# Performance work log

Measured on AMD Instinct MI355X. Metric: run time of the kernel, lower is better.

## Reference

```python
import jax, jax.numpy as jnp
import numpy as np

B, Hdim, Wdim, C = 8, 128, 128, 64
HEADS, R, EXP = 1, 8, 4
HID = C * EXP
EPS = 1e-5

def layernorm(x, g, b):
    m = jnp.mean(x, -1, keepdims=True)
    v = jnp.mean((x - m) ** 2, -1, keepdims=True)
    return (x - m) * jax.lax.rsqrt(v + EPS) * g + b

def setup_inputs() -> dict:
    key = jax.random.key(0)
    ks = jax.random.split(key, 16)
    s = 0.02
    inp = {
        'x': jax.random.normal(ks[0], (B, Hdim * Wdim, C), jnp.float32),
        'H': Hdim, 'W': Wdim,
        'ln1_g': jnp.ones((C,)), 'ln1_b': jnp.zeros((C,)),
        'q_w': jax.random.normal(ks[1], (C, C)) * s, 'q_b': jnp.zeros((C,)),
        'kv_w': jax.random.normal(ks[2], (C, 2 * C)) * s, 'kv_b': jnp.zeros((2 * C,)),
        'proj_w': jax.random.normal(ks[3], (C, C)) * s, 'proj_b': jnp.zeros((C,)),
        'sr_w': jax.random.normal(ks[4], (R, R, C, C)) * s, 'sr_b': jnp.zeros((C,)),
        'srn_g': jnp.ones((C,)), 'srn_b': jnp.zeros((C,)),
        'ln2_g': jnp.ones((C,)), 'ln2_b': jnp.zeros((C,)),
        'fc1_w': jax.random.normal(ks[5], (C, HID)) * s, 'fc1_b': jnp.zeros((HID,)),
        'dw_w': jax.random.normal(ks[6], (3, 3, 1, HID)) * s,  # depthwise HWIO
        'fc2_w': jax.random.normal(ks[7], (HID, C)) * s, 'fc2_b': jnp.zeros((C,)),
    }
    return inp

def reference(x, H, W, ln1_g, ln1_b, q_w, q_b, kv_w, kv_b, proj_w, proj_b,
              sr_w, sr_b, srn_g, srn_b, ln2_g, ln2_b, fc1_w, fc1_b, dw_w, fc2_w, fc2_b):
    Bq, N, Cq = x.shape
    hd = Cq // HEADS
    scale = hd ** -0.5
    # --- attention branch (dropout = identity in eval) ---
    h = layernorm(x, ln1_g, ln1_b)
    q = (h @ q_w + q_b).reshape(Bq, N, HEADS, hd)
    # spatial reduction: conv RxR stride R
    xr = h.reshape(Bq, H, W, Cq)
    xr = jax.lax.conv_general_dilated(xr, sr_w, (R, R), 'VALID',
                                      dimension_numbers=('NHWC', 'HWIO', 'NHWC')) + sr_b
    Nr = (H // R) * (W // R)
    xr = layernorm(xr.reshape(Bq, Nr, Cq), srn_g, srn_b)
    kv = (xr @ kv_w + kv_b).reshape(Bq, Nr, 2, HEADS, hd)
    k, v = kv[:, :, 0], kv[:, :, 1]  # [B,Nr,H,hd]
    attn = jnp.einsum('bnhd,bmhd->bhnm', q, k) * scale
    attn = jax.nn.softmax(attn, axis=-1)
    o = jnp.einsum('bhnm,bmhd->bnhd', attn, v).reshape(Bq, N, Cq)
    x = x + (o @ proj_w + proj_b)
    # --- Mix-FFN branch ---
    h2 = layernorm(x, ln2_g, ln2_b)
    f = h2 @ fc1_w + fc1_b  # [B,N,HID]
    f = f.reshape(Bq, H, W, HID)
    f = jax.lax.conv_general_dilated(f, dw_w, (1, 1), 'SAME',
                                     dimension_numbers=('NHWC', 'HWIO', 'NHWC'),
                                     feature_group_count=HID)
    f = jax.nn.gelu(f.reshape(Bq, N, HID), approximate=False)
    return x + (f @ fc2_w + fc2_b)
```

## Files before the change

kernel.cpp:

```cpp
#include <hip/hip_runtime.h>
#include <hip/hip_bf16.h>


typedef __hip_bfloat16 bf16;
typedef __attribute__((ext_vector_type(8))) short s8v;
typedef __attribute__((ext_vector_type(4))) float f4v;

#define N_TOK 16384
#define CDIM 64
#define NR 256
#define HID 256
#define EPS 1e-5f

__device__ __forceinline__ float b2f(bf16 v) { return __bfloat162float(v); }
__device__ __forceinline__ bf16 f2b(float v) { return __float2bfloat16(v); }
__device__ __forceinline__ short bfbits(float f) {
  bf16 h = __float2bfloat16(f);
  return __builtin_bit_cast(short, h);
}
__device__ __forceinline__ float bits2f(short s) {
  const unsigned u = ((unsigned)(unsigned short)s) << 16;
  return __builtin_bit_cast(float, u);
}
__device__ __forceinline__ float2 unpk(unsigned u) {
  const unsigned lo = u << 16;
  const unsigned hi = u & 0xffff0000u;
  float2 r;
  r.x = __builtin_bit_cast(float, lo);
  r.y = __builtin_bit_cast(float, hi);
  return r;
}

__device__ __forceinline__ float wred_sum(float v) {
#pragma unroll
  for (int o = 32; o >= 1; o >>= 1) v += __shfl_xor(v, o);
  return v;
}

__global__ __launch_bounds__(256) void k_prep(
    const float* __restrict__ qw, const float* __restrict__ pw,
    const float* __restrict__ w1, const float* __restrict__ w2,
    const float* __restrict__ srw,
    bf16* __restrict__ qwT, bf16* __restrict__ pwT,
    bf16* __restrict__ w1T, bf16* __restrict__ w2T,
    bf16* __restrict__ srwT) {
  int id = blockIdx.x * 256 + threadIdx.x;
  if (id < 4096) {
    const int n = id >> 6, k = id & 63;
    qwT[(n << 6) + ((((k >> 3) ^ (n & 7)) << 3)) + (k & 7)] = f2b(qw[(k << 6) + n]);
  } else if (id < 8192) {
    id -= 4096;
    const int n = id >> 6, k = id & 63;
    pwT[(n << 6) + ((((k >> 3) ^ (n & 7)) << 3)) + (k & 7)] = f2b(pw[(k << 6) + n]);
  } else if (id < 24576) {
    id -= 8192;
    const int n = id >> 6, k = id & 63;
    w1T[(n << 6) + ((((k >> 3) ^ (n & 7)) << 3)) + (k & 7)] = f2b(w1[(k << 8) + n]);
  } else if (id < 40960) {
    id -= 24576;
    const int n = id >> 8, k = id & 255;
    w2T[(n << 8) + ((((k >> 3) ^ (n & 7)) << 3)) + (k & 7)] = f2b(w2[(k << 6) + n]);
  } else {
    id -= 40960;
    const int n = id >> 12, k = id & 4095;
    srwT[(n << 12) + k] = f2b(srw[(k << 6) + n]);
  }
}

__global__ __launch_bounds__(256) void k_ln1(
    const float* __restrict__ x, const float* __restrict__ g, const float* __restrict__ bb,
    bf16* __restrict__ h) {
  const int tid = threadIdx.x;
  const int row = (blockIdx.x << 6) + (tid >> 2), q4 = tid & 3;
  const float4* xp = (const float4*)(x + (((size_t)row) << 6) + (q4 << 4));
  float v[16];
#pragma unroll
  for (int j4 = 0; j4 < 4; j4++) {
    const float4 a = xp[j4];
    v[j4 * 4 + 0] = a.x; v[j4 * 4 + 1] = a.y; v[j4 * 4 + 2] = a.z; v[j4 * 4 + 3] = a.w;
  }
  float s = 0.f;
#pragma unroll
  for (int j = 0; j < 16; j++) s += v[j];
  s += __shfl_xor(s, 1); s += __shfl_xor(s, 2);
  const float mean = s * (1.f / 64.f);
  float vs = 0.f;
#pragma unroll
  for (int j = 0; j < 16; j++) { v[j] -= mean; vs += v[j] * v[j]; }
  vs += __shfl_xor(vs, 1); vs += __shfl_xor(vs, 2);
  const float rs = rsqrtf(vs * (1.f / 64.f) + EPS);
  s8v p0, p1;
#pragma unroll
  for (int j = 0; j < 16; j++) {
    const int c = (q4 << 4) + j;
    const short hb = bfbits(v[j] * rs * g[c] + bb[c]);
    if (j < 8) p0[j] = hb; else p1[j - 8] = hb;
  }
  bf16* hp = h + (((size_t)row) << 6) + (q4 << 4);
  *(s8v*)hp = p0;
  *(s8v*)(hp + 8) = p1;
}

__global__ __launch_bounds__(256) void k_srgemm(
    const bf16* __restrict__ h, const bf16* __restrict__ srwT,
    float* __restrict__ part) {
  const int tid = threadIdx.x, lane = tid & 63, wv = tid >> 6;
  const int quad = lane >> 4, li = lane & 15;
  const int rt = blockIdx.x >> 3, ks = blockIdx.x & 7;
  const int g = (rt << 6) + (wv << 4) + li;
  const int b = g >> 8, pm = g & 255;
  const int py = pm >> 4, px = pm & 15;
  const int n0 = (py << 10) + (px << 3);
  const size_t abase = ((size_t)(b * N_TOK + n0)) << 6;

  f4v acc[4];
#pragma unroll
  for (int t = 0; t < 4; t++) acc[t] = (f4v){0.f, 0.f, 0.f, 0.f};

#pragma unroll
  for (int i = 0; i < 16; i++) {
    const int kk = (ks << 4) + i;
    const int sp = kk >> 1;
    const int nd = ((sp >> 3) << 7) + (sp & 7);
    const int ci = ((kk & 1) << 5) + (quad << 3);
    s8v av = *(const s8v*)(h + abase + (((size_t)nd) << 6) + ci);
    const int koff = (kk << 5) + (quad << 3);
#pragma unroll
    for (int t = 0; t < 4; t++) {
      s8v bv = *(const s8v*)(srwT + ((((t << 4) + li)) << 12) + koff);
      acc[t] = __builtin_amdgcn_mfma_f32_16x16x32_bf16(av, bv, acc[t], 0, 0, 0);
    }
  }
  float* pp = part + (((size_t)ks) << 17);
#pragma unroll
  for (int t = 0; t < 4; t++)
#pragma unroll
    for (int r = 0; r < 4; r++) {
      const int row = (rt << 6) + (wv << 4) + (quad << 2) + r;
      pp[(row << 6) + (t << 4) + li] = acc[t][r];
    }
}

__global__ __launch_bounds__(256) void k_kv(
    const float* __restrict__ part, const float* __restrict__ srb,
    const float* __restrict__ sng, const float* __restrict__ snb,
    const float* __restrict__ kvw, const float* __restrict__ kvb,
    bf16* __restrict__ kbuf, bf16* __restrict__ vbufT) {
  const int tid = threadIdx.x, co = tid & 63, wv = tid >> 6;
  const int tok = (blockIdx.x << 2) + wv;
  float acc = srb[co];
#pragma unroll
  for (int s = 0; s < 8; s++) acc += part[(((size_t)s) << 17) + (tok << 6) + co];
  const float mean = wred_sum(acc) * (1.f / 64.f);
  const float d = acc - mean;
  const float var = wred_sum(d * d) * (1.f / 64.f);
  const float xn = d * rsqrtf(var + EPS) * sng[co] + snb[co];
  float ka = kvb[co];
  float va = kvb[64 + co];
#pragma unroll
  for (int ci = 0; ci < 64; ci++) {
    const float xv = __shfl(xn, ci);
    ka += xv * kvw[ci * 128 + co];
    va += xv * kvw[ci * 128 + 64 + co];
  }
  const int b = tok >> 8, nr = tok & 255;
  kbuf[(tok << 6) + co] = f2b(ka);
  vbufT[((((size_t)b << 6) + co) << 8) + nr] = f2b(va);
}

__global__ __launch_bounds__(256) void k_attn(
    const bf16* __restrict__ h, const float* __restrict__ x,
    const bf16* __restrict__ qwT, const float* __restrict__ qb,
    const bf16* __restrict__ kbuf, const bf16* __restrict__ vbufT,
    const bf16* __restrict__ pwT, const float* __restrict__ pb,
    bf16* __restrict__ x2) {
  __shared__ __align__(16) short lds[36864];
  const int tid = threadIdx.x, lane = tid & 63, wv = tid >> 6;
  const int quad = lane >> 4, li = lane & 15;
  const int b = blockIdx.x >> 8;
  const int rowbase = ((blockIdx.x & 255) << 6) + (wv << 4);

#pragma unroll
  for (int it = 0; it < 8; it++) {
    const int idx = (it << 8) + tid;
    {
      const int row = idx >> 3, c8 = idx & 7;
      uint4 d = *(const uint4*)(kbuf + (((size_t)(b * 256 + row)) << 6) + (c8 << 3));
      *(uint4*)&lds[(row << 6) + ((c8 ^ (row & 7)) << 3)] = d;
    }
    {
      const int row = idx >> 5, c8 = idx & 31;
      uint4 d = *(const uint4*)(vbufT + (((size_t)(b * 64 + row)) << 8) + (c8 << 3));
      *(uint4*)&lds[16384 + (row << 8) + ((c8 ^ (row & 7)) << 3)] = d;
    }
  }

  s8v qwf[2][4];
#pragma unroll
  for (int s = 0; s < 2; s++)
#pragma unroll
    for (int t = 0; t < 4; t++) {
      const int n = (t << 4) + li;
      qwf[s][t] = *(const s8v*)(qwT + (n << 6) + ((((s << 2) + quad) ^ (n & 7)) << 3));
    }

  const size_t hbase = (((size_t)(b * N_TOK + rowbase + li)) << 6) + (quad << 3);
  s8v ha[2];
  ha[0] = *(const s8v*)(h + hbase);
  ha[1] = *(const s8v*)(h + hbase + 32);

  f4v qacc[4];
#pragma unroll
  for (int t = 0; t < 4; t++) {
    const float bv = qb[(t << 4) + li];
    qacc[t] = (f4v){bv, bv, bv, bv};
  }
#pragma unroll
  for (int s = 0; s < 2; s++)
#pragma unroll
    for (int t = 0; t < 4; t++)
      qacc[t] = __builtin_amdgcn_mfma_f32_16x16x32_bf16(ha[s], qwf[s][t], qacc[t], 0, 0, 0);

  const int qoff = 32768 + (wv << 10);
#pragma unroll
  for (int t = 0; t < 4; t++)
#pragma unroll
    for (int r = 0; r < 4; r++) {
      const int m = (quad << 2) + r, c = (t << 4) + li;
      lds[qoff + (m << 6) + ((((c >> 3) ^ (m & 7)) << 3)) + (c & 7)] = bfbits(qacc[t][r] * 0.125f);
    }
  __syncthreads();

  s8v qa[2];
#pragma unroll
  for (int s = 0; s < 2; s++)
    qa[s] = *(const s8v*)&lds[qoff + (li << 6) + ((((s << 2) + quad) ^ (li & 7)) << 3)];

  f4v sv[16];
#pragma unroll
  for (int t = 0; t < 16; t++) sv[t] = (f4v){0.f, 0.f, 0.f, 0.f};
#pragma unroll
  for (int t = 0; t < 16; t++)
#pragma unroll
    for (int s = 0; s < 2; s++) {
      s8v kb = *(const s8v*)&lds[(((t << 4) + li) << 6) + ((((s << 2) + quad) ^ (li & 7)) << 3)];
      sv[t] = __builtin_amdgcn_mfma_f32_16x16x32_bf16(qa[s], kb, sv[t], 0, 0, 0);
    }

  float rl[4];
#pragma unroll
  for (int r = 0; r < 4; r++) {
    float mx = -1e30f;
#pragma unroll
    for (int t = 0; t < 16; t++) mx = fmaxf(mx, sv[t][r]);
#pragma unroll
    for (int o = 1; o <= 8; o <<= 1) mx = fmaxf(mx, __shfl_xor(mx, o));
    float sm = 0.f;
#pragma unroll
    for (int t = 0; t < 16; t++) {
      const float e = __expf(sv[t][r] - mx);
      sv[t][r] = e;
      sm += e;
    }
#pragma unroll
    for (int o = 1; o <= 8; o <<= 1) sm += __shfl_xor(sm, o);
    rl[r] = 1.0f / sm;
  }
  __syncthreads();

  const int poff = wv << 12;
#pragma unroll
  for (int t = 0; t < 16; t++)
#pragma unroll
    for (int r = 0; r < 4; r++) {
      const int m = (quad << 2) + r, c = (t << 4) + li;
      lds[poff + (m << 8) + (((c >> 3) ^ (m & 7)) << 3) + (c & 7)] = bfbits(sv[t][r]);
    }

  f4v oacc[4];
#pragma unroll
  for (int t = 0; t < 4; t++) oacc[t] = (f4v){0.f, 0.f, 0.f, 0.f};
#pragma unroll
  for (int s = 0; s < 8; s++) {
    s8v pa = *(const s8v*)&lds[poff + (li << 8) + ((((s << 2) + quad) ^ (li & 7)) << 3)];
#pragma unroll
    for (int t = 0; t < 4; t++) {
      s8v vb = *(const s8v*)&lds[16384 + (((t << 4) + li) << 8) + ((((s << 2) + quad) ^ (li & 7)) << 3)];
      oacc[t] = __builtin_amdgcn_mfma_f32_16x16x32_bf16(pa, vb, oacc[t], 0, 0, 0);
    }
  }

#pragma unroll
  for (int t = 0; t < 4; t++)
#pragma unroll
    for (int r = 0; r < 4; r++) {
      const int m = (quad << 2) + r, c = (t << 4) + li;
      lds[qoff + (m << 6) + (((c >> 3) ^ (m & 7)) << 3) + (c & 7)] = bfbits(oacc[t][r] * rl[r]);
    }
  s8v oa[2];
#pragma unroll
  for (int s = 0; s < 2; s++)
    oa[s] = *(const s8v*)&lds[qoff + (li << 6) + ((((s << 2) + quad) ^ (li & 7)) << 3)];

  f4v pacc[4];
#pragma unroll
  for (int t = 0; t < 4; t++) {
    const float bv = pb[(t << 4) + li];
    pacc[t] = (f4v){bv, bv, bv, bv};
  }
#pragma unroll
  for (int s = 0; s < 2; s++)
#pragma unroll
    for (int t = 0; t < 4; t++) {
      const int n = (t << 4) + li;
      s8v wf = *(const s8v*)(pwT + (n << 6) + ((((s << 2) + quad) ^ (n & 7)) << 3));
      pacc[t] = __builtin_amdgcn_mfma_f32_16x16x32_bf16(oa[s], wf, pacc[t], 0, 0, 0);
    }
#pragma unroll
  for (int t = 0; t < 4; t++)
#pragma unroll
    for (int r = 0; r < 4; r++) {
      const size_t gi = (((size_t)(b * N_TOK + rowbase + (quad << 2) + r)) << 6) + (t << 4) + li;
      x2[gi] = f2b(x[gi] + pacc[t][r]);
    }
}

__global__ __launch_bounds__(256) void k_fc1(
    const bf16* __restrict__ x2, const float* __restrict__ g, const float* __restrict__ bb,
    const bf16* __restrict__ w1T, const float* __restrict__ b1,
    bf16* __restrict__ f) {
  __shared__ __align__(16) short hs[4096];
  const int tid = threadIdx.x, lane = tid & 63, wv = tid >> 6;
  const int quad = lane >> 4, li = lane & 15;
  const int r0 = blockIdx.x << 6;

  s8v wf[2][4];
  float bv[4];
#pragma unroll
  for (int t = 0; t < 4; t++) {
    const int n = (((wv << 2) + t) << 4) + li;
    bv[t] = b1[n];
#pragma unroll
    for (int s = 0; s < 2; s++)
      wf[s][t] = *(const s8v*)(w1T + (n << 6) + ((((s << 2) + quad) ^ (n & 7)) << 3));
  }

  const int row = tid >> 2, q4 = tid & 3;
  const bf16* xp = x2 + (((size_t)(r0 + row)) << 6) + (q4 << 4);
  s8v xa = *(const s8v*)xp;
  s8v xb = *(const s8v*)(xp + 8);
  float v[16];
#pragma unroll
  for (int j = 0; j < 8; j++) {
    v[j] = bits2f(xa[j]);
    v[8 + j] = bits2f(xb[j]);
  }
  float s = 0.f;
#pragma unroll
  for (int j = 0; j < 16; j++) s += v[j];
  s += __shfl_xor(s, 1); s += __shfl_xor(s, 2);
  const float mean = s * (1.f / 64.f);
  float vs = 0.f;
#pragma unroll
  for (int j = 0; j < 16; j++) { v[j] -= mean; vs += v[j] * v[j]; }
  vs += __shfl_xor(vs, 1); vs += __shfl_xor(vs, 2);
  const float rs = rsqrtf(vs * (1.f / 64.f) + EPS);
  s8v p0, p1;
#pragma unroll
  for (int j = 0; j < 16; j++) {
    const int c = (q4 << 4) + j;
    const short hb = bfbits(v[j] * rs * g[c] + bb[c]);
    if (j < 8) p0[j] = hb; else p1[j - 8] = hb;
  }
  {
    const int m7 = row & 7;
    *(s8v*)&hs[(row << 6) + (((q4 << 1) ^ m7) << 3)] = p0;
    *(s8v*)&hs[(row << 6) + ((((q4 << 1) + 1) ^ m7) << 3)] = p1;
  }
  __syncthreads();

  s8v qa[4][2];
#pragma unroll
  for (int rg = 0; rg < 4; rg++) {
    const int m = (rg << 4) + li;
#pragma unroll
    for (int s2 = 0; s2 < 2; s2++)
      qa[rg][s2] = *(const s8v*)&hs[(m << 6) + ((((s2 << 2) + quad) ^ (m & 7)) << 3)];
  }
  f4v acc[4][4];
#pragma unroll
  for (int rg = 0; rg < 4; rg++)
#pragma unroll
    for (int t = 0; t < 4; t++) acc[rg][t] = (f4v){bv[t], bv[t], bv[t], bv[t]};
#pragma unroll
  for (int rg = 0; rg < 4; rg++)
#pragma unroll
    for (int t = 0; t < 4; t++) {
      acc[rg][t] = __builtin_amdgcn_mfma_f32_16x16x32_bf16(qa[rg][0], wf[0][t], acc[rg][t], 0, 0, 0);
      acc[rg][t] = __builtin_amdgcn_mfma_f32_16x16x32_bf16(qa[rg][1], wf[1][t], acc[rg][t], 0, 0, 0);
    }
#pragma unroll
  for (int rg = 0; rg < 4; rg++)
#pragma unroll
    for (int t = 0; t < 4; t++)
#pragma unroll
      for (int r = 0; r < 4; r++) {
        const int rr = r0 + (rg << 4) + (quad << 2) + r;
        f[((size_t)rr << 8) + ((((wv << 2) + t) << 4)) + li] = f2b(acc[rg][t][r]);
      }
}

__global__ __launch_bounds__(256) void k_out(
    const bf16* __restrict__ f, const float* __restrict__ dww,
    const bf16* __restrict__ x2, const bf16* __restrict__ w2T,
    const float* __restrict__ fc2b, float* __restrict__ out) {
  __shared__ __align__(16) short gs[16384];
  const int tid = threadIdx.x, lane = tid & 63, wv = tid >> 6;
  const int quad = lane >> 4, li = lane & 15;
  const int b = blockIdx.x >> 8;
  const int y = (blockIdx.x >> 1) & 127;
  const int xh = blockIdx.x & 1;

  const int tg = tid & 15, cg = tid >> 4;
  float2 acc[4][8];
#pragma unroll
  for (int t = 0; t < 4; t++)
#pragma unroll
    for (int j = 0; j < 8; j++) acc[t][j] = (float2){0.f, 0.f};

  const int x0 = (xh << 6) + (tg << 2);
  for (int dy = 0; dy < 3; dy++) {
    const int yy = y + dy - 1;
    if (yy < 0 || yy > 127) continue;
    float2 dwr[3][8];
#pragma unroll
    for (int dx = 0; dx < 3; dx++) {
      const float4* wp = (const float4*)(dww + (dy * 3 + dx) * HID + (cg << 4));
#pragma unroll
      for (int j4 = 0; j4 < 4; j4++) {
        const float4 w4 = wp[j4];
        dwr[dx][j4 * 2 + 0] = (float2){w4.x, w4.y};
        dwr[dx][j4 * 2 + 1] = (float2){w4.z, w4.w};
      }
    }
#pragma unroll
    for (int xi = -1; xi <= 4; xi++) {
      const int xx = x0 + xi;
      if (xx < 0 || xx > 127) continue;
      const bf16* fp = f + (((((size_t)(b * 128 + yy)) << 7) + xx) << 8) + (cg << 4);
      const uint4 ua = *(const uint4*)fp;
      const uint4 ub = *(const uint4*)(fp + 8);
      float2 fv[8];
      fv[0] = unpk(ua.x); fv[1] = unpk(ua.y); fv[2] = unpk(ua.z); fv[3] = unpk(ua.w);
      fv[4] = unpk(ub.x); fv[5] = unpk(ub.y); fv[6] = unpk(ub.z); fv[7] = unpk(ub.w);
#pragma unroll
      for (int dx = 0; dx < 3; dx++) {
        const int t = xi - dx + 1;
        if (t < 0 || t > 3) continue;
#pragma unroll
        for (int j = 0; j < 8; j++) {
          acc[t][j].x += fv[j].x * dwr[dx][j].x;
          acc[t][j].y += fv[j].y * dwr[dx][j].y;
        }
      }
    }
  }

#pragma unroll
  for (int t = 0; t < 4; t++) {
    const int m = (tg << 2) + t;
    s8v p0, p1;
#pragma unroll
    for (int j = 0; j < 8; j++) {
      const float a0 = acc[t][j].x, a1 = acc[t][j].y;
      const float g0 = 0.5f * a0 * (1.f + erff(a0 * 0.70710678118654752f));
      const float g1 = 0.5f * a1 * (1.f + erff(a1 * 0.70710678118654752f));
      if (j < 4) { p0[2 * j] = bfbits(g0); p0[2 * j + 1] = bfbits(g1); }
      else       { p1[2 * (j - 4)] = bfbits(g0); p1[2 * (j - 4) + 1] = bfbits(g1); }
    }
    const int m7 = m & 7;
    *(s8v*)&gs[(m << 8) + (((cg << 1) ^ m7) << 3)] = p0;
    *(s8v*)&gs[(m << 8) + ((((cg << 1) + 1) ^ m7) << 3)] = p1;
  }
  __syncthreads();

  f4v oa2[4];
#pragma unroll
  for (int ct = 0; ct < 4; ct++) {
    const float bb2 = fc2b[(ct << 4) + li];
    oa2[ct] = (f4v){bb2, bb2, bb2, bb2};
  }
  const int m = (wv << 4) + li;
#pragma unroll
  for (int kc = 0; kc < 8; kc++) {
    const int ch = (kc << 2) + quad;
    s8v av = *(const s8v*)&gs[(m << 8) + ((ch ^ (m & 7)) << 3)];
#pragma unroll
    for (int ct = 0; ct < 4; ct++) {
      const int n = (ct << 4) + li;
      s8v bv2 = *(const s8v*)(w2T + (n << 8) + ((ch ^ (n & 7)) << 3));
      oa2[ct] = __builtin_amdgcn_mfma_f32_16x16x32_bf16(av, bv2, oa2[ct], 0, 0, 0);
    }
  }
  const int tokbase = (b << 14) + (y << 7) + (xh << 6) + (wv << 4) + (quad << 2);
#pragma unroll
  for (int ct = 0; ct < 4; ct++)
#pragma unroll
    for (int r = 0; r < 4; r++) {
      const size_t gi = (((size_t)(tokbase + r)) << 6) + (ct << 4) + li;
      out[gi] = b2f(x2[gi]) + oa2[ct][r];
    }
}

extern "C" void kernel_launch(void* const* d_in, const int* in_sizes, int n_in,
                              void* d_out, int out_size, void* d_ws, size_t ws_size,
                              hipStream_t stream) {
  const float* x    = (const float*)d_in[0];
  const float* ln1g = (const float*)d_in[3];
  const float* ln1b = (const float*)d_in[4];
  const float* qw   = (const float*)d_in[5];
  const float* qb   = (const float*)d_in[6];
  const float* kvw  = (const float*)d_in[7];
  const float* kvb  = (const float*)d_in[8];
  const float* pw   = (const float*)d_in[9];
  const float* pb   = (const float*)d_in[10];
  const float* srw  = (const float*)d_in[11];
  const float* srb  = (const float*)d_in[12];
  const float* sng  = (const float*)d_in[13];
  const float* snb  = (const float*)d_in[14];
  const float* ln2g = (const float*)d_in[15];
  const float* ln2b = (const float*)d_in[16];
  const float* w1   = (const float*)d_in[17];
  const float* b1   = (const float*)d_in[18];
  const float* dww  = (const float*)d_in[19];
  const float* w2   = (const float*)d_in[20];
  const float* b2v  = (const float*)d_in[21];
  float* out = (float*)d_out;

  char* ws = (char*)d_ws;
  bf16*  x2    = (bf16*)ws;
  bf16*  h     = (bf16*)(ws + 16777216);
  bf16*  kbuf  = (bf16*)(ws + 33554432);
  bf16*  vbufT = (bf16*)(ws + 33816576);
  bf16*  fbuf  = (bf16*)(ws + 34078720);
  bf16*  w1T   = (bf16*)(ws + 101187584);
  bf16*  w2T   = (bf16*)(ws + 101220352);
  bf16*  qwT   = (bf16*)(ws + 101253120);
  bf16*  pwT   = (bf16*)(ws + 101261312);
  bf16*  srwT  = (bf16*)(ws + 101269504);
  float* part  = (float*)(ws + 101793792);

  k_prep  <<< 1184, 256, 0, stream>>>(qw, pw, w1, w2, srw, qwT, pwT, w1T, w2T, srwT);
  k_ln1   <<< 2048, 256, 0, stream>>>(x, ln1g, ln1b, h);
  k_srgemm<<<  256, 256, 0, stream>>>(h, srwT, part);
  k_kv    <<<  512, 256, 0, stream>>>(part, srb, sng, snb, kvw, kvb, kbuf, vbufT);
  k_attn  <<< 2048, 256, 0, stream>>>(h, x, qwT, qb, kbuf, vbufT, pwT, pb, x2);
  k_fc1   <<< 2048, 256, 0, stream>>>(x2, ln2g, ln2b, w1T, b1, fbuf);
  k_out   <<< 2048, 256, 0, stream>>>(fbuf, dww, x2, w2T, b2v, out);
}
```

Baseline: 263.3 us.

## Cut LDS and register pressure in attention and depthwise kernels, deepen sr split-K

The attention kernel no longer stages V in shared memory and instead reads V fragments straight from global memory. This shrinks the LDS footprint from about 72KB to about 40KB so more blocks can fit per CU. Query-weight fragments are loaded inline next to each MFMA rather than held in registers up front, and the depthwise conv + GELU kernel now processes its 16 channels in two passes of 8 to lower register use. The spatial-reduction GEMM doubles its split-K factor to 16 and launches 512 blocks, which doubles the partial-sum buffer and the reduction work in k_kv. The trade-off is extra global/L2 traffic for V in attention and a larger partial buffer in the workspace.

```diff
diff --git a/kernel.cpp b/kernel.cpp
--- a/kernel.cpp
+++ b/kernel.cpp
@@ -106,7 +106,7 @@
     float* __restrict__ part) {
   const int tid = threadIdx.x, lane = tid & 63, wv = tid >> 6;
   const int quad = lane >> 4, li = lane & 15;
-  const int rt = blockIdx.x >> 3, ks = blockIdx.x & 7;
+  const int rt = blockIdx.x >> 4, ks = blockIdx.x & 15;
   const int g = (rt << 6) + (wv << 4) + li;
   const int b = g >> 8, pm = g & 255;
   const int py = pm >> 4, px = pm & 15;
@@ -118,8 +118,8 @@
   for (int t = 0; t < 4; t++) acc[t] = (f4v){0.f, 0.f, 0.f, 0.f};
 
 #pragma unroll
-  for (int i = 0; i < 16; i++) {
-    const int kk = (ks << 4) + i;
+  for (int i = 0; i < 8; i++) {
+    const int kk = (ks << 3) + i;
     const int sp = kk >> 1;
     const int nd = ((sp >> 3) << 7) + (sp & 7);
     const int ci = ((kk & 1) << 5) + (quad << 3);
@@ -150,7 +150,7 @@
   const int tok = (blockIdx.x << 2) + wv;
   float acc = srb[co];
 #pragma unroll
-  for (int s = 0; s < 8; s++) acc += part[(((size_t)s) << 17) + (tok << 6) + co];
+  for (int s = 0; s < 16; s++) acc += part[(((size_t)s) << 17) + (tok << 6) + co];
   const float mean = wred_sum(acc) * (1.f / 64.f);
   const float d = acc - mean;
   const float var = wred_sum(d * d) * (1.f / 64.f);
@@ -174,7 +174,7 @@
     const bf16* __restrict__ kbuf, const bf16* __restrict__ vbufT,
     const bf16* __restrict__ pwT, const float* __restrict__ pb,
     bf16* __restrict__ x2) {
-  __shared__ __align__(16) short lds[36864];
+  __shared__ __align__(16) short lds[20480];
   const int tid = threadIdx.x, lane = tid & 63, wv = tid >> 6;
   const int quad = lane >> 4, li = lane & 15;
   const int b = blockIdx.x >> 8;
@@ -183,26 +183,10 @@
 #pragma unroll
   for (int it = 0; it < 8; it++) {
     const int idx = (it << 8) + tid;
-    {
-      const int row = idx >> 3, c8 = idx & 7;
-      uint4 d = *(const uint4*)(kbuf + (((size_t)(b * 256 + row)) << 6) + (c8 << 3));
-      *(uint4*)&lds[(row << 6) + ((c8 ^ (row & 7)) << 3)] = d;
-    }
-    {
-      const int row = idx >> 5, c8 = idx & 31;
-      uint4 d = *(const uint4*)(vbufT + (((size_t)(b * 64 + row)) << 8) + (c8 << 3));
-      *(uint4*)&lds[16384 + (row << 8) + ((c8 ^ (row & 7)) << 3)] = d;
-    }
-  }
-
-  s8v qwf[2][4];
-#pragma unroll
-  for (int s = 0; s < 2; s++)
-#pragma unroll
-    for (int t = 0; t < 4; t++) {
-      const int n = (t << 4) + li;
-      qwf[s][t] = *(const s8v*)(qwT + (n << 6) + ((((s << 2) + quad) ^ (n & 7)) << 3));
-    }
+    const int row = idx >> 3, c8 = idx & 7;
+    uint4 d = *(const uint4*)(kbuf + (((size_t)(b * 256 + row)) << 6) + (c8 << 3));
+    *(uint4*)&lds[(row << 6) + ((c8 ^ (row & 7)) << 3)] = d;
+  }
 
   const size_t hbase = (((size_t)(b * N_TOK + rowbase + li)) << 6) + (quad << 3);
   s8v ha[2];
@@ -218,10 +202,13 @@
 #pragma unroll
   for (int s = 0; s < 2; s++)
 #pragma unroll
-    for (int t = 0; t < 4; t++)
-      qacc[t] = __builtin_amdgcn_mfma_f32_16x16x32_bf16(ha[s], qwf[s][t], qacc[t], 0, 0, 0);
-
-  const int qoff = 32768 + (wv << 10);
+    for (int t = 0; t < 4; t++) {
+      const int n = (t << 4) + li;
+      s8v qwf = *(const s8v*)(qwT + (n << 6) + ((((s << 2) + quad) ^ (n & 7)) << 3));
+      qacc[t] = __builtin_amdgcn_mfma_f32_16x16x32_bf16(ha[s], qwf, qacc[t], 0, 0, 0);
+    }
+
+  const int qoff = 16384 + (wv << 10);
 #pragma unroll
   for (int t = 0; t < 4; t++)
 #pragma unroll
@@ -285,7 +272,7 @@
     s8v pa = *(const s8v*)&lds[poff + (li << 8) + ((((s << 2) + quad) ^ (li & 7)) << 3)];
 #pragma unroll
     for (int t = 0; t < 4; t++) {
-      s8v vb = *(const s8v*)&lds[16384 + (((t << 4) + li) << 8) + ((((s << 2) + quad) ^ (li & 7)) << 3)];
+      s8v vb = *(const s8v*)(vbufT + (((size_t)(b * 64 + (t << 4) + li)) << 8) + (s << 5) + (quad << 3));
       oacc[t] = __builtin_amdgcn_mfma_f32_16x16x32_bf16(pa, vb, oacc[t], 0, 0, 0);
     }
   }
@@ -422,65 +409,63 @@
   const int xh = blockIdx.x & 1;
 
   const int tg = tid & 15, cg = tid >> 4;
-  float2 acc[4][8];
-#pragma unroll
-  for (int t = 0; t < 4; t++)
-#pragma unroll
-    for (int j = 0; j < 8; j++) acc[t][j] = (float2){0.f, 0.f};
-
   const int x0 = (xh << 6) + (tg << 2);
-  for (int dy = 0; dy < 3; dy++) {
-    const int yy = y + dy - 1;
-    if (yy < 0 || yy > 127) continue;
-    float2 dwr[3][8];
-#pragma unroll
-    for (int dx = 0; dx < 3; dx++) {
-      const float4* wp = (const float4*)(dww + (dy * 3 + dx) * HID + (cg << 4));
-#pragma unroll
-      for (int j4 = 0; j4 < 4; j4++) {
-        const float4 w4 = wp[j4];
-        dwr[dx][j4 * 2 + 0] = (float2){w4.x, w4.y};
-        dwr[dx][j4 * 2 + 1] = (float2){w4.z, w4.w};
+
+#pragma unroll 1
+  for (int p = 0; p < 2; p++) {
+    const int ch0 = (p << 7) + (cg << 3);
+    float2 acc[4][4];
+#pragma unroll
+    for (int t = 0; t < 4; t++)
+#pragma unroll
+      for (int j = 0; j < 4; j++) acc[t][j] = (float2){0.f, 0.f};
+
+    for (int dy = 0; dy < 3; dy++) {
+      const int yy = y + dy - 1;
+      if (yy < 0 || yy > 127) continue;
+      float2 dwr[3][4];
+#pragma unroll
+      for (int dx = 0; dx < 3; dx++) {
+        const float4* wp = (const float4*)(dww + (dy * 3 + dx) * HID + ch0);
+        const float4 wa = wp[0], wb = wp[1];
+        dwr[dx][0] = (float2){wa.x, wa.y};
+        dwr[dx][1] = (float2){wa.z, wa.w};
+        dwr[dx][2] = (float2){wb.x, wb.y};
+        dwr[dx][3] = (float2){wb.z, wb.w};
       }
-    }
-#pragma unroll
-    for (int xi = -1; xi <= 4; xi++) {
-      const int xx = x0 + xi;
-      if (xx < 0 || xx > 127) continue;
-      const bf16* fp = f + (((((size_t)(b * 128 + yy)) << 7) + xx) << 8) + (cg << 4);
-      const uint4 ua = *(const uint4*)fp;
-      const uint4 ub = *(const uint4*)(fp + 8);
-      float2 fv[8];
-      fv[0] = unpk(ua.x); fv[1] = unpk(ua.y); fv[2] = unpk(ua.z); fv[3] = unpk(ua.w);
-      fv[4] = unpk(ub.x); fv[5] = unpk(ub.y); fv[6] = unpk(ub.z); fv[7] = unpk(ub.w);
-#pragma unroll
-      for (int dx = 0; dx < 3; dx++) {
-        const int t = xi - dx + 1;
-        if (t < 0 || t > 3) continue;
-#pragma unroll
-        for (int j = 0; j < 8; j++) {
-          acc[t][j].x += fv[j].x * dwr[dx][j].x;
-          acc[t][j].y += fv[j].y * dwr[dx][j].y;
+#pragma unroll
+      for (int xi = -1; xi <= 4; xi++) {
+        const int xx = x0 + xi;
+        if (xx < 0 || xx > 127) continue;
+        const uint4 ua = *(const uint4*)(f + (((((size_t)(b * 128 + yy)) << 7) + xx) << 8) + ch0);
+        float2 fv[4];
+        fv[0] = unpk(ua.x); fv[1] = unpk(ua.y); fv[2] = unpk(ua.z); fv[3] = unpk(ua.w);
+#pragma unroll
+        for (int dx = 0; dx < 3; dx++) {
+          const int t = xi - dx + 1;
+          if (t < 0 || t > 3) continue;
+#pragma unroll
+          for (int j = 0; j < 4; j++) {
+            acc[t][j].x += fv[j].x * dwr[dx][j].x;
+            acc[t][j].y += fv[j].y * dwr[dx][j].y;
+          }
         }
       }
     }
-  }
-
-#pragma unroll
-  for (int t = 0; t < 4; t++) {
-    const int m = (tg << 2) + t;
-    s8v p0, p1;
-#pragma unroll
-    for (int j = 0; j < 8; j++) {
-      const float a0 = acc[t][j].x, a1 = acc[t][j].y;
-      const float g0 = 0.5f * a0 * (1.f + erff(a0 * 0.70710678118654752f));
-      const float g1 = 0.5f * a1 * (1.f + erff(a1 * 0.70710678118654752f));
-      if (j < 4) { p0[2 * j] = bfbits(g0); p0[2 * j + 1] = bfbits(g1); }
-      else       { p1[2 * (j - 4)] = bfbits(g0); p1[2 * (j - 4) + 1] = bfbits(g1); }
-    }
-    const int m7 = m & 7;
-    *(s8v*)&gs[(m << 8) + (((cg << 1) ^ m7) << 3)] = p0;
-    *(s8v*)&gs[(m << 8) + ((((cg << 1) + 1) ^ m7) << 3)] = p1;
+
+    const int c8 = cg + (p << 4);
+#pragma unroll
+    for (int t = 0; t < 4; t++) {
+      const int m = (tg << 2) + t;
+      s8v pk;
+#pragma unroll
+      for (int j = 0; j < 4; j++) {
+        const float a0 = acc[t][j].x, a1 = acc[t][j].y;
+        pk[2 * j]     = bfbits(0.5f * a0 * (1.f + erff(a0 * 0.70710678118654752f)));
+        pk[2 * j + 1] = bfbits(0.5f * a1 * (1.f + erff(a1 * 0.70710678118654752f)));
+      }
+      *(s8v*)&gs[(m << 8) + ((c8 ^ (m & 7)) << 3)] = pk;
+    }
   }
   __syncthreads();
 
@@ -552,7 +537,7 @@
 
   k_prep  <<< 1184, 256, 0, stream>>>(qw, pw, w1, w2, srw, qwT, pwT, w1T, w2T, srwT);
   k_ln1   <<< 2048, 256, 0, stream>>>(x, ln1g, ln1b, h);
-  k_srgemm<<<  256, 256, 0, stream>>>(h, srwT, part);
+  k_srgemm<<<  512, 256, 0, stream>>>(h, srwT, part);
   k_kv    <<<  512, 256, 0, stream>>>(part, srb, sng, snb, kvw, kvb, kbuf, vbufT);
   k_attn  <<< 2048, 256, 0, stream>>>(h, x, qwT, qb, kbuf, vbufT, pwT, pb, x2);
   k_fc1   <<< 2048, 256, 0, stream>>>(x2, ln2g, ln2b, w1T, b1, fbuf);
```

Measured after the change: 274.5 us. 4.3% more time.
